# Kernel optimization log

Measured on AMD Instinct MI355X. Metric: run time of the kernel, lower is better.

The kernel has to match this reference:

```python
import jax, jax.numpy as jnp
import numpy as np

B, DEC, F = 64, 12, 32        # batch, decoder steps, decoder feature size
L, H = 2, 512                 # gru layers, hidden size
E, T = 96, 4                  # encoder seq len, target size


def gru_cell(x, h, Wi, Wh, bi, bh):
    # PyTorch GRUCell math
    gi = x @ Wi.T + bi
    gh = h @ Wh.T + bh
    i_r, i_z, i_n = jnp.split(gi, 3, axis=-1)
    h_r, h_z, h_n = jnp.split(gh, 3, axis=-1)
    r = jax.nn.sigmoid(i_r + h_r)
    z = jax.nn.sigmoid(i_z + h_z)
    n = jnp.tanh(i_n + r * h_n)
    return (1.0 - z) * n + z * h


def setup_inputs() -> dict:
    key = jax.random.key(0)
    ks = jax.random.split(key, 12)
    s = lambda k, shape: jax.random.normal(k, shape, jnp.float32) * 0.02
    return {
        "inputs": jax.random.normal(ks[0], (B, DEC, F), jnp.float32),
        "hidden": jax.random.normal(ks[1], (L, B, H), jnp.float32) * 0.1,
        "enc_outputs": jax.random.normal(ks[2], (B, E, H), jnp.float32),
        "target_indices": jnp.arange(T, dtype=jnp.int32),
        "W_attn": s(ks[3], (H, 2 * H)),
        "b_attn": jnp.zeros((H,), jnp.float32),
        "v_attn": s(ks[4], (H,)),
        "gru_Wi0": s(ks[5], (3 * H, F + H)),
        "gru_Wh0": s(ks[6], (3 * H, H)),
        "gru_bi0": jnp.zeros((3 * H,), jnp.float32),
        "gru_bh0": jnp.zeros((3 * H,), jnp.float32),
        "gru_Wi1": s(ks[7], (3 * H, H)),
        "gru_Wh1": s(ks[8], (3 * H, H)),
        "gru_bi1": jnp.zeros((3 * H,), jnp.float32),
        "gru_bh1": jnp.zeros((3 * H,), jnp.float32),
        "W_out": s(ks[9], (T, 2 * H + F)),
        "b_out": jnp.zeros((T,), jnp.float32),
    }


def reference(inputs, hidden, enc_outputs, target_indices,
              W_attn, b_attn, v_attn,
              gru_Wi0, gru_Wh0, gru_bi0, gru_bh0,
              gru_Wi1, gru_Wh1, gru_bi1, gru_bh1,
              W_out, b_out):
    Hs = hidden.shape[-1]
    Wa_h, Wa_e = W_attn[:, :Hs], W_attn[:, Hs:]
    # encoder projection of the attn linear is constant over timesteps
    enc_proj = jnp.einsum('beh,gh->beg', enc_outputs, Wa_e)  # [B,E,H]
    layers = ((gru_Wi0, gru_Wh0, gru_bi0, gru_bh0),
              (gru_Wi1, gru_Wh1, gru_bi1, gru_bh1))

    def step(carry, x_t):
        h, cur = carry                     # h: [L,B,H], cur: [B,F]
        hl = h[-1]                         # final-layer hidden [B,H]
        energy = jnp.tanh(enc_proj + (hl @ Wa_h.T + b_attn)[:, None, :])
        w = jax.nn.softmax(energy @ v_attn, axis=1)          # [B,E]
        ws = jnp.einsum('be,beh->bh', w, enc_outputs)        # [B,H]
        x = jnp.concatenate([cur, ws], axis=-1)              # [B,F+H]
        new_h = []
        for l, (Wi, Wh, bi, bh) in enumerate(layers):
            hn = gru_cell(x, h[l], Wi, Wh, bi, bh)
            new_h.append(hn)
            x = hn
        out = jnp.concatenate([x, ws, cur], axis=-1) @ W_out.T + b_out  # [B,T]
        nxt = x_t.at[:, target_indices].set(out)  # feed prediction back
        return (jnp.stack(new_h), nxt), out

    xs = jnp.swapaxes(inputs, 0, 1)  # [DEC,B,F]
    (_, _), outs = jax.lax.scan(step, (hidden, inputs[:, 0, :]), xs)
    return jnp.swapaxes(outs, 0, 1)  # [B,DEC,T]
```

## Files before the change

kernel.cpp:

```cpp
#include <hip/hip_runtime.h>
#include <hip/hip_fp16.h>

#define NB   64
#define NDEC 12
#define NF   32
#define NH   512
#define NE   96
#define NT   4
#define KI0  (NF + NH)
#define KOUT (2*NH + NF)

typedef _Float16 half8_t __attribute__((ext_vector_type(8)));
typedef float   float4_t __attribute__((ext_vector_type(4)));

__device__ __forceinline__ float fast_tanh(float x) {
    x = fminf(fmaxf(x, -15.f), 15.f);
    float e = __expf(2.f * x);
    return (e - 1.f) / (e + 1.f);
}
__device__ __forceinline__ float fast_sig(float x) {
    return 1.f / (1.f + __expf(-x));
}

__global__ __launch_bounds__(256) void k_prep(
    const float* __restrict__ Wi0, const float* __restrict__ Wh0,
    const float* __restrict__ Wi1, const float* __restrict__ Wh1,
    const float* __restrict__ Wout, const float* __restrict__ Wattn,
    const float* __restrict__ hidden, const float* __restrict__ inputs,
    __half* __restrict__ Wi0h, __half* __restrict__ Wh0h,
    __half* __restrict__ Wi1h, __half* __restrict__ Wh1h,
    __half* __restrict__ Wouth, __half* __restrict__ WahH,
    __half* __restrict__ WaeH,
    float* __restrict__ h0row, float* __restrict__ h1row,
    __half* __restrict__ h0h, __half* __restrict__ h1h,
    __half* __restrict__ xcat_h)
{
    int i = blockIdx.x*256 + threadIdx.x;
    const int n0 = 1536*KI0, n1 = 1536*512, n4 = 4*KOUT, n5 = 512*512;
    if (i < n0) { Wi0h[i] = __float2half_rn(Wi0[i]); return; }  i -= n0;
    if (i < n1) { Wh0h[i] = __float2half_rn(Wh0[i]); return; }  i -= n1;
    if (i < n1) { Wi1h[i] = __float2half_rn(Wi1[i]); return; }  i -= n1;
    if (i < n1) { Wh1h[i] = __float2half_rn(Wh1[i]); return; }  i -= n1;
    if (i < n4) { Wouth[i] = __float2half_rn(Wout[i]); return; } i -= n4;
    if (i < n5) {
        int g = i >> 9, k = i & 511;
        WahH[i] = __float2half_rn(Wattn[(size_t)g*1024 + k]);
        return;
    }
    i -= n5;
    if (i < n5) {
        int g = i >> 9, k = i & 511;
        WaeH[i] = __float2half_rn(Wattn[(size_t)g*1024 + 512 + k]);
        return;
    }
    i -= n5;
    if (i < NB*NH) {
        int b = i >> 9, k = i & 511;
        float v0 = hidden[b*NH + k];
        float v1 = hidden[NB*NH + b*NH + k];
        h0row[b*NH + k] = v0;  h0h[b*NH + k] = __float2half_rn(v0);
        h1row[b*NH + k] = v1;  h1h[b*NH + k] = __float2half_rn(v1);
        return;
    }
    i -= NB*NH;
    if (i < NB*NF) {
        int b = i >> 5, k = i & 31;
        xcat_h[(size_t)b*KI0 + k] = __float2half_rn(inputs[b*NDEC*NF + k]);
    }
}

__global__ __launch_bounds__(256) void k_encproj(const float* __restrict__ enc,
                                                 const __half* __restrict__ WaeH,
                                                 __half* __restrict__ encph) {
    int x = blockIdx.x;
    int by = x >> 3, bx = x & 7;
    int t = threadIdx.x, w = t >> 6, lane = t & 63;
    int mr = lane & 15, kq = lane >> 4;
    int m = by*64 + w*16 + mr;
    const float* arow = enc + (size_t)m*NH;
    float4_t acc[4] = {{0.f,0.f,0.f,0.f},{0.f,0.f,0.f,0.f},
                       {0.f,0.f,0.f,0.f},{0.f,0.f,0.f,0.f}};
    for (int kb = 0; kb < NH; kb += 32) {
        int k = kb + kq*8;
        float4 a0 = *(const float4*)(arow + k);
        float4 a1 = *(const float4*)(arow + k + 4);
        half8_t a;
        a[0] = (_Float16)a0.x; a[1] = (_Float16)a0.y;
        a[2] = (_Float16)a0.z; a[3] = (_Float16)a0.w;
        a[4] = (_Float16)a1.x; a[5] = (_Float16)a1.y;
        a[6] = (_Float16)a1.z; a[7] = (_Float16)a1.w;
        #pragma unroll
        for (int j = 0; j < 4; ++j) {
            int n = bx*64 + j*16 + mr;
            half8_t b = *(const half8_t*)(WaeH + (size_t)n*NH + k);
            acc[j] = __builtin_amdgcn_mfma_f32_16x16x32_f16(a, b, acc[j], 0, 0, 0);
        }
    }
    #pragma unroll
    for (int j = 0; j < 4; ++j) {
        int col = bx*64 + j*16 + mr;
        #pragma unroll
        for (int r = 0; r < 4; ++r) {
            int row = by*64 + w*16 + kq*4 + r;
            encph[(size_t)row*NH + col] = __float2half_rn(acc[j][r]);
        }
    }
}

__global__ __launch_bounds__(256) void k_gemA(
    const float* __restrict__ inputs, const int* __restrict__ tgt,
    const __half* __restrict__ WahH, const float* __restrict__ battn,
    const __half* __restrict__ Wouth, const float* __restrict__ bout,
    const __half* __restrict__ Wh0h, const __half* __restrict__ Wh1h,
    const __half* __restrict__ h0h, const __half* __restrict__ h1h,
    __half* __restrict__ xcat_h,
    float* __restrict__ attcT,
    float* __restrict__ ghb,
    float* __restrict__ out,
    int s, int att_on)
{
    int blk = blockIdx.x, t = threadIdx.x;
    int w = t >> 6, lane = t & 63;
    int mr = lane & 15, kq = lane >> 4;
    int gA = att_on ? 896 : 0;
    __shared__ float parts[4][16][17];

    if (blk < gA) {
        int sblk = (blk & 7)*112 + (blk >> 3);
        const __half* arow;
        const __half* brow;
        float* gdst = nullptr;
        int is_att = 0, rt16 = 0, b0 = 0;
        if (sblk < 128) {
            int rt = sblk >> 2, bq = sblk & 3;
            rt16 = rt*16; b0 = bq*16;
            arow = WahH + (size_t)(rt16 + mr)*NH;
            brow = h1h + (size_t)(b0 + mr)*NH;
            is_att = 1;
        } else {
            int gw = sblk - 128;
            int rt = gw >> 2, bq = gw & 3;
            int layer = (rt >= 96) ? 1 : 0;
            int rloc = (rt - layer*96) * 16;
            const __half* Wh = layer ? Wh1h : Wh0h;
            const __half* Xh = layer ? h1h : h0h;
            arow = Wh + (size_t)(rloc + mr)*NH;
            brow = Xh + (size_t)(bq*16 + mr)*NH;
            gdst = ghb + ((size_t)layer*3*NH + rloc)*NB + bq*16;
        }
        float bat = is_att ? battn[rt16 + (t & 15)] : 0.f;
        int kb0 = w*128 + kq*8;
        half8_t a0 = *(const half8_t*)(arow + kb0);
        half8_t b0v = *(const half8_t*)(brow + kb0);
        half8_t a1 = *(const half8_t*)(arow + kb0 + 32);
        half8_t b1 = *(const half8_t*)(brow + kb0 + 32);
        half8_t a2 = *(const half8_t*)(arow + kb0 + 64);
        half8_t b2 = *(const half8_t*)(brow + kb0 + 64);
        half8_t a3 = *(const half8_t*)(arow + kb0 + 96);
        half8_t b3 = *(const half8_t*)(brow + kb0 + 96);
        float4_t acc = {0.f,0.f,0.f,0.f};
        acc = __builtin_amdgcn_mfma_f32_16x16x32_f16(a0, b0v, acc, 0, 0, 0);
        acc = __builtin_amdgcn_mfma_f32_16x16x32_f16(a1, b1, acc, 0, 0, 0);
        acc = __builtin_amdgcn_mfma_f32_16x16x32_f16(a2, b2, acc, 0, 0, 0);
        acc = __builtin_amdgcn_mfma_f32_16x16x32_f16(a3, b3, acc, 0, 0, 0);
        #pragma unroll
        for (int r = 0; r < 4; ++r) parts[w][kq*4 + r][mr] = acc[r];
        __syncthreads();
        if (is_att) {
            int jl = t & 15, bl = t >> 4;
            float v = parts[0][jl][bl] + parts[1][jl][bl]
                    + parts[2][jl][bl] + parts[3][jl][bl];
            attcT[(size_t)(b0 + bl)*NH + rt16 + jl] = v + bat;
        } else {
            int jl = t >> 4, bl = t & 15;
            float v = parts[0][jl][bl] + parts[1][jl][bl]
                    + parts[2][jl][bl] + parts[3][jl][bl];
            gdst[(size_t)jl*NB + bl] = v;
        }
        return;
    }

    if (s == 0) return;
    int bq = w;
    int b = bq*16 + mr;
    const __half* h1b = h1h + (size_t)b*NH;
    const __half* xcb = xcat_h + (size_t)b*KI0;
    int ar = (mr < 4) ? mr : 3;
    const __half* arow = Wouth + (size_t)ar*KOUT;
    float4_t acc = {0.f,0.f,0.f,0.f};
    for (int kb = 0; kb < KOUT; kb += 32) {
        int k = kb + kq*8;
        half8_t a = *(const half8_t*)(arow + k);
        const __half* bp = (k < NH)   ? (h1b + k)
                         : (k < 2*NH) ? (xcb + NF + (k - NH))
                                      : (xcb + (k - 2*NH));
        half8_t bb = *(const half8_t*)bp;
        acc = __builtin_amdgcn_mfma_f32_16x16x32_f16(a, bb, acc, 0, 0, 0);
    }
    float o0 = __shfl(acc[0], mr) + bout[0];
    float o1 = __shfl(acc[1], mr) + bout[1];
    float o2 = __shfl(acc[2], mr) + bout[2];
    float o3 = __shfl(acc[3], mr) + bout[3];
    if (kq == 0) {
        *(float4*)(out + (size_t)b*(NDEC*NT) + (s-1)*NT) = make_float4(o0,o1,o2,o3);
    }
    if (s < NDEC) {
        int t0 = tgt[0], t1 = tgt[1], t2 = tgt[2], t3 = tgt[3];
        const float* ip = inputs + (size_t)b*(NDEC*NF) + (s-1)*NF;
        half8_t hv;
        #pragma unroll
        for (int i = 0; i < 8; ++i) {
            int f = kq*8 + i;
            float v = ip[f];
            v = (f == t0) ? o0 : (f == t1) ? o1 : (f == t2) ? o2 : (f == t3) ? o3 : v;
            hv[i] = (_Float16)__float2half_rn(v);
        }
        *(half8_t*)(xcat_h + (size_t)b*KI0 + kq*8) = hv;
    }
}

__global__ __launch_bounds__(1024) void k_soft(
    const float* __restrict__ vattn,
    const float* __restrict__ attcT,
    const __half* __restrict__ encph, const float* __restrict__ enc,
    __half* __restrict__ xcat_h)
{
    int b = blockIdx.x, t = threadIdx.x;
    int lane = t & 63, widx = t >> 6;
    __shared__ float vs[NH], atts[NH];
    __shared__ float pes[NE], combA[NH], combB[NH];
    __shared__ float invD_sh;

    if (t < NH) { vs[t] = vattn[t]; atts[t] = attcT[(size_t)b*NH + t]; }

    float er[48];
    {
        int k = t & 511, half = t >> 9;
        const float* eb = enc + ((size_t)b*NE + half*48)*NH + k;
        #pragma unroll
        for (int e = 0; e < 48; ++e) er[e] = eb[(size_t)e*NH];
    }
    __syncthreads();

    {
        float ar[8], vr[8];
        #pragma unroll
        for (int i = 0; i < 8; ++i) { ar[i] = atts[lane*8 + i]; vr[i] = vs[lane*8 + i]; }
        for (int it = 0; it < 6; ++it) {
            int e = widx + it*16;
            const __half* ep = encph + ((size_t)(b*NE + e))*NH + lane*8;
            uint4 u = *(const uint4*)ep;
            __half2 p0 = *(__half2*)&u.x, p1 = *(__half2*)&u.y;
            __half2 p2 = *(__half2*)&u.z, p3 = *(__half2*)&u.w;
            float2 f0 = __half22float2(p0), f1 = __half22float2(p1);
            float2 f2 = __half22float2(p2), f3 = __half22float2(p3);
            float sacc;
            sacc  = fast_tanh(f0.x + ar[0]) * vr[0];
            sacc += fast_tanh(f0.y + ar[1]) * vr[1];
            sacc += fast_tanh(f1.x + ar[2]) * vr[2];
            sacc += fast_tanh(f1.y + ar[3]) * vr[3];
            sacc += fast_tanh(f2.x + ar[4]) * vr[4];
            sacc += fast_tanh(f2.y + ar[5]) * vr[5];
            sacc += fast_tanh(f3.x + ar[6]) * vr[6];
            sacc += fast_tanh(f3.y + ar[7]) * vr[7];
            #pragma unroll
            for (int off = 32; off; off >>= 1) sacc += __shfl_down(sacc, off);
            if (lane == 0) pes[e] = __expf(sacc);
        }
    }
    __syncthreads();

    if (t < 64) {
        float v = pes[t] + ((t < 32) ? pes[64 + t] : 0.f);
        #pragma unroll
        for (int off = 32; off; off >>= 1) v += __shfl_down(v, off);
        if (t == 0) invD_sh = 1.f / v;
    }
    __syncthreads();

    {
        int k = t & 511, half = t >> 9;
        float acc = 0.f;
        #pragma unroll
        for (int e = 0; e < 48; ++e) acc += pes[half*48 + e] * er[e];
        if (half == 0) combA[k] = acc; else combB[k] = acc;
    }
    __syncthreads();
    if (t < NH) {
        float v = (combA[t] + combB[t]) * invD_sh;
        xcat_h[(size_t)b*KI0 + NF + t] = __float2half_rn(v);
    }
}

__global__ __launch_bounds__(768) void k_gru(
    const __half* __restrict__ Wi,
    const float* __restrict__ bi, const float* __restrict__ bh,
    const __half* __restrict__ xh, int K,
    const float* __restrict__ ghbL,
    const float* __restrict__ hold,
    float* __restrict__ hnew,
    __half* __restrict__ hnewh)
{
    int blk = blockIdx.x, t = threadIdx.x;
    int w = t >> 6, lane = t & 63;
    int mr = lane & 15, kq = lane >> 4;
    int sblk = (blk & 7)*16 + (blk >> 3);
    int jg = sblk >> 2, bq = sblk & 3;
    int j0 = jg*16, b0 = bq*16;
    __shared__ float parts[3][4][16][17];

    float ghr = 0.f, ghz = 0.f, ghn = 0.f, hp = 0.f;
    float biR = 0.f, bhR = 0.f, biZ = 0.f, bhZ = 0.f, biN = 0.f, bhN = 0.f;
    if (t < 256) {
        int jl = t >> 4, bl = t & 15;
        int j = j0 + jl, b = b0 + bl;
        ghr = ghbL[(size_t)(0*NH + j)*NB + b];
        ghz = ghbL[(size_t)(1*NH + j)*NB + b];
        ghn = ghbL[(size_t)(2*NH + j)*NB + b];
        hp  = hold[(size_t)b*NH + j];
        biR = bi[j];        bhR = bh[j];
        biZ = bi[NH + j];   bhZ = bh[NH + j];
        biN = bi[2*NH + j]; bhN = bh[2*NH + j];
    }

    int gate = w >> 2, c = w & 3;
    int nsteps = K >> 5;
    int rem = nsteps & 3;
    int base = c*(nsteps >> 2) + ((c < rem) ? c : rem);
    int cnt  = (nsteps >> 2) + ((c < rem) ? 1 : 0);
    const __half* arow = Wi + (size_t)(gate*NH + j0 + mr)*K;
    const __half* brow = xh + (size_t)(b0 + mr)*K;
    float4_t acc = {0.f,0.f,0.f,0.f};
    for (int i2 = 0; i2 < cnt; ++i2) {
        int kb = (base + i2)*32;
        half8_t a = *(const half8_t*)(arow + kb + kq*8);
        half8_t b = *(const half8_t*)(brow + kb + kq*8);
        acc = __builtin_amdgcn_mfma_f32_16x16x32_f16(a, b, acc, 0, 0, 0);
    }
    #pragma unroll
    for (int r = 0; r < 4; ++r) parts[gate][c][kq*4 + r][mr] = acc[r];
    __syncthreads();

    if (t < 256) {
        int jl = t >> 4, bl = t & 15;
        int j = j0 + jl, b = b0 + bl;
        float S0 = parts[0][0][jl][bl] + parts[0][1][jl][bl]
                 + parts[0][2][jl][bl] + parts[0][3][jl][bl];
        float S1 = parts[1][0][jl][bl] + parts[1][1][jl][bl]
                 + parts[1][2][jl][bl] + parts[1][3][jl][bl];
        float S2 = parts[2][0][jl][bl] + parts[2][1][jl][bl]
                 + parts[2][2][jl][bl] + parts[2][3][jl][bl];
        float r = fast_sig(S0 + ghr + biR + bhR);
        float z = fast_sig(S1 + ghz + biZ + bhZ);
        float n = fast_tanh(S2 + biN + r*(ghn + bhN));
        float hv = (1.f - z)*n + z*hp;
        hnew[(size_t)b*NH + j] = hv;
        hnewh[(size_t)b*NH + j] = __float2half_rn(hv);
    }
}

extern "C" void kernel_launch(void* const* d_in, const int* in_sizes, int n_in,
                              void* d_out, int out_size, void* d_ws, size_t ws_size,
                              hipStream_t stream) {
    const float* inputs = (const float*)d_in[0];
    const float* hidden = (const float*)d_in[1];
    const float* enc    = (const float*)d_in[2];
    const int*   tgt    = (const int*)d_in[3];
    const float* Wattn  = (const float*)d_in[4];
    const float* battn  = (const float*)d_in[5];
    const float* vattn  = (const float*)d_in[6];
    const float* Wi0    = (const float*)d_in[7];
    const float* Wh0    = (const float*)d_in[8];
    const float* bi0    = (const float*)d_in[9];
    const float* bh0    = (const float*)d_in[10];
    const float* Wi1    = (const float*)d_in[11];
    const float* Wh1    = (const float*)d_in[12];
    const float* bi1    = (const float*)d_in[13];
    const float* bh1    = (const float*)d_in[14];
    const float* Wout   = (const float*)d_in[15];
    const float* bout   = (const float*)d_in[16];
    float* out = (float*)d_out;

    float* h0row  = (float*)d_ws;
    float* h1row  = h0row + NB*NH;
    float* ghb    = h1row + NB*NH;
    float* attcT  = ghb + 2*3*NH*NB;
    __half* Wi0h  = (__half*)(attcT + NB*NH);
    __half* Wh0h  = Wi0h + 1536*KI0;
    __half* Wi1h  = Wh0h + 1536*NH;
    __half* Wh1h  = Wi1h + 1536*NH;
    __half* Wouth = Wh1h + 1536*NH;
    __half* WahH  = Wouth + 4*KOUT;
    __half* WaeH  = WahH + NH*NH;
    __half* h0h   = WaeH + NH*NH;
    __half* h1h   = h0h + NB*NH;
    __half* xcat_h= h1h + NB*NH;
    __half* encph = xcat_h + NB*KI0;

    const int prep_n = 1536*KI0 + 3*1536*NH + 4*KOUT + 2*NH*NH + NB*NH + NB*NF;
    k_prep<<<(prep_n + 255)/256, 256, 0, stream>>>(
        Wi0, Wh0, Wi1, Wh1, Wout, Wattn, hidden, inputs,
        Wi0h, Wh0h, Wi1h, Wh1h, Wouth, WahH, WaeH,
        h0row, h1row, h0h, h1h, xcat_h);
    k_encproj<<<768, 256, 0, stream>>>(enc, WaeH, encph);

    for (int s = 0; s < NDEC; ++s) {
        k_gemA<<<(s == 0) ? 896 : 897, 256, 0, stream>>>(
            inputs, tgt, WahH, battn, Wouth, bout, Wh0h, Wh1h,
            h0h, h1h, xcat_h, attcT, ghb, out, s, 1);
        k_soft<<<NB, 1024, 0, stream>>>(vattn, attcT, encph, enc, xcat_h);
        k_gru<<<128, 768, 0, stream>>>(Wi0h, bi0, bh0,
                                       xcat_h, KI0,
                                       ghb,
                                       h0row, h0row, h0h);
        k_gru<<<128, 768, 0, stream>>>(Wi1h, bi1, bh1,
                                       h0h, NH,
                                       ghb + 3*NH*NB,
                                       h1row, h1row, h1h);
    }
    k_gemA<<<1, 256, 0, stream>>>(
        inputs, tgt, WahH, battn, Wouth, bout, Wh0h, Wh1h,
        h0h, h1h, xcat_h, attcT, ghb, out, NDEC, 0);
}
```

Measured before the change: 533.4 us.

## Move hidden-gate GEMMs and output head into softmax kernel with double-buffered xcat

The per-step work is rebalanced across kernels. The attention projection becomes its own small 32-block kernel. The recurrent gate GEMMs (Wh·h) and the output/feedback block now run as extra blocks inside the softmax kernel, so they overlap with the attention softmax. xcat is double-buffered so the output head can read the previous step's concatenated input while the softmax blocks write the current one. The critical path gets shorter, at the cost of an extra launch and 1024-thread blocks doing small GEMM tiles.

```diff
diff --git a/kernel.cpp b/kernel.cpp
--- a/kernel.cpp
+++ b/kernel.cpp
@@ -33,7 +33,7 @@
     __half* __restrict__ WaeH,
     float* __restrict__ h0row, float* __restrict__ h1row,
     __half* __restrict__ h0h, __half* __restrict__ h1h,
-    __half* __restrict__ xcat_h)
+    __half* __restrict__ xcat0)
 {
     int i = blockIdx.x*256 + threadIdx.x;
     const int n0 = 1536*KI0, n1 = 1536*512, n4 = 4*KOUT, n5 = 512*512;
@@ -65,7 +65,7 @@
     i -= NB*NH;
     if (i < NB*NF) {
         int b = i >> 5, k = i & 31;
-        xcat_h[(size_t)b*KI0 + k] = __float2half_rn(inputs[b*NDEC*NF + k]);
+        xcat0[(size_t)b*KI0 + k] = __float2half_rn(inputs[b*NDEC*NF + k]);
     }
 }
 
@@ -107,51 +107,81 @@
     }
 }
 
-__global__ __launch_bounds__(256) void k_gemA(
-    const float* __restrict__ inputs, const int* __restrict__ tgt,
+__global__ __launch_bounds__(1024) void k_att(
     const __half* __restrict__ WahH, const float* __restrict__ battn,
-    const __half* __restrict__ Wouth, const float* __restrict__ bout,
-    const __half* __restrict__ Wh0h, const __half* __restrict__ Wh1h,
-    const __half* __restrict__ h0h, const __half* __restrict__ h1h,
-    __half* __restrict__ xcat_h,
-    float* __restrict__ attcT,
-    float* __restrict__ ghb,
-    float* __restrict__ out,
-    int s, int att_on)
+    const __half* __restrict__ h1h,
+    float* __restrict__ attcT)
 {
     int blk = blockIdx.x, t = threadIdx.x;
     int w = t >> 6, lane = t & 63;
     int mr = lane & 15, kq = lane >> 4;
-    int gA = att_on ? 896 : 0;
-    __shared__ float parts[4][16][17];
-
-    if (blk < gA) {
-        int sblk = (blk & 7)*112 + (blk >> 3);
-        const __half* arow;
-        const __half* brow;
-        float* gdst = nullptr;
-        int is_att = 0, rt16 = 0, b0 = 0;
-        if (sblk < 128) {
-            int rt = sblk >> 2, bq = sblk & 3;
-            rt16 = rt*16; b0 = bq*16;
-            arow = WahH + (size_t)(rt16 + mr)*NH;
-            brow = h1h + (size_t)(b0 + mr)*NH;
-            is_att = 1;
-        } else {
-            int gw = sblk - 128;
-            int rt = gw >> 2, bq = gw & 3;
-            int layer = (rt >= 96) ? 1 : 0;
-            int rloc = (rt - layer*96) * 16;
-            const __half* Wh = layer ? Wh1h : Wh0h;
-            const __half* Xh = layer ? h1h : h0h;
-            arow = Wh + (size_t)(rloc + mr)*NH;
-            brow = Xh + (size_t)(bq*16 + mr)*NH;
-            gdst = ghb + ((size_t)layer*3*NH + rloc)*NB + bq*16;
-        }
-        float bat = is_att ? battn[rt16 + (t & 15)] : 0.f;
-        int kb0 = w*128 + kq*8;
+    int rt = (blk & 7)*4 + (blk >> 3);
+    int rt16 = rt*16;
+    int bq = w >> 2, wq = w & 3;
+    __shared__ float parts[4][4][16][17];
+
+    float bat = battn[rt16 + (t & 15)];
+    const __half* arow = WahH + (size_t)(rt16 + mr)*NH;
+    const __half* brow = h1h + (size_t)(bq*16 + mr)*NH;
+    int kb0 = wq*128 + kq*8;
+    half8_t a0 = *(const half8_t*)(arow + kb0);
+    half8_t b0 = *(const half8_t*)(brow + kb0);
+    half8_t a1 = *(const half8_t*)(arow + kb0 + 32);
+    half8_t b1 = *(const half8_t*)(brow + kb0 + 32);
+    half8_t a2 = *(const half8_t*)(arow + kb0 + 64);
+    half8_t b2 = *(const half8_t*)(brow + kb0 + 64);
+    half8_t a3 = *(const half8_t*)(arow + kb0 + 96);
+    half8_t b3 = *(const half8_t*)(brow + kb0 + 96);
+    float4_t acc = {0.f,0.f,0.f,0.f};
+    acc = __builtin_amdgcn_mfma_f32_16x16x32_f16(a0, b0, acc, 0, 0, 0);
+    acc = __builtin_amdgcn_mfma_f32_16x16x32_f16(a1, b1, acc, 0, 0, 0);
+    acc = __builtin_amdgcn_mfma_f32_16x16x32_f16(a2, b2, acc, 0, 0, 0);
+    acc = __builtin_amdgcn_mfma_f32_16x16x32_f16(a3, b3, acc, 0, 0, 0);
+    #pragma unroll
+    for (int r = 0; r < 4; ++r) parts[bq][wq][kq*4 + r][mr] = acc[r];
+    __syncthreads();
+
+    int sub = t >> 8, tt = t & 255;
+    int jl = tt & 15, bl = tt >> 4;
+    float v = parts[sub][0][jl][bl] + parts[sub][1][jl][bl]
+            + parts[sub][2][jl][bl] + parts[sub][3][jl][bl];
+    attcT[(size_t)(sub*16 + bl)*NH + rt16 + jl] = v + bat;
+}
+
+__global__ __launch_bounds__(1024) void k_soft(
+    const float* __restrict__ inputs, const int* __restrict__ tgt,
+    const float* __restrict__ vattn,
+    const float* __restrict__ attcT,
+    const __half* __restrict__ encph, const float* __restrict__ enc,
+    const __half* __restrict__ Wouth, const float* __restrict__ bout,
+    const __half* __restrict__ Wh0h, const __half* __restrict__ Wh1h,
+    const __half* __restrict__ h0h, const __half* __restrict__ h1h,
+    float* __restrict__ ghb,
+    const __half* __restrict__ xcatP,
+    __half* __restrict__ xcatC,
+    float* __restrict__ out, int s)
+{
+    int blk = blockIdx.x, t = threadIdx.x;
+    int lane = t & 63, widx = t >> 6;
+    __shared__ float vs[NH], atts[NH];
+    __shared__ float pes[NE], combA[NH], combB[NH];
+    __shared__ float invD_sh;
+    __shared__ float parts[4][4][16][17];
+
+    if (blk >= 64 && blk < 256) {
+        int gblk = blk - 64;
+        int rt = (gblk & 7)*24 + (gblk >> 3);
+        int layer = (rt >= 96) ? 1 : 0;
+        int rloc = (rt - layer*96) * 16;
+        int bq = widx >> 2, wq = widx & 3;
+        int mr = lane & 15, kq = lane >> 4;
+        const __half* Wh = layer ? Wh1h : Wh0h;
+        const __half* Xh = layer ? h1h : h0h;
+        const __half* arow = Wh + (size_t)(rloc + mr)*NH;
+        const __half* brow = Xh + (size_t)(bq*16 + mr)*NH;
+        int kb0 = wq*128 + kq*8;
         half8_t a0 = *(const half8_t*)(arow + kb0);
-        half8_t b0v = *(const half8_t*)(brow + kb0);
+        half8_t b0 = *(const half8_t*)(brow + kb0);
         half8_t a1 = *(const half8_t*)(arow + kb0 + 32);
         half8_t b1 = *(const half8_t*)(brow + kb0 + 32);
         half8_t a2 = *(const half8_t*)(arow + kb0 + 64);
@@ -159,52 +189,46 @@
         half8_t a3 = *(const half8_t*)(arow + kb0 + 96);
         half8_t b3 = *(const half8_t*)(brow + kb0 + 96);
         float4_t acc = {0.f,0.f,0.f,0.f};
-        acc = __builtin_amdgcn_mfma_f32_16x16x32_f16(a0, b0v, acc, 0, 0, 0);
+        acc = __builtin_amdgcn_mfma_f32_16x16x32_f16(a0, b0, acc, 0, 0, 0);
         acc = __builtin_amdgcn_mfma_f32_16x16x32_f16(a1, b1, acc, 0, 0, 0);
         acc = __builtin_amdgcn_mfma_f32_16x16x32_f16(a2, b2, acc, 0, 0, 0);
         acc = __builtin_amdgcn_mfma_f32_16x16x32_f16(a3, b3, acc, 0, 0, 0);
         #pragma unroll
-        for (int r = 0; r < 4; ++r) parts[w][kq*4 + r][mr] = acc[r];
+        for (int r = 0; r < 4; ++r) parts[bq][wq][kq*4 + r][mr] = acc[r];
         __syncthreads();
-        if (is_att) {
-            int jl = t & 15, bl = t >> 4;
-            float v = parts[0][jl][bl] + parts[1][jl][bl]
-                    + parts[2][jl][bl] + parts[3][jl][bl];
-            attcT[(size_t)(b0 + bl)*NH + rt16 + jl] = v + bat;
-        } else {
-            int jl = t >> 4, bl = t & 15;
-            float v = parts[0][jl][bl] + parts[1][jl][bl]
-                    + parts[2][jl][bl] + parts[3][jl][bl];
-            gdst[(size_t)jl*NB + bl] = v;
-        }
+        int sub = t >> 8, tt = t & 255;
+        int jl = tt >> 4, bl = tt & 15;
+        float v = parts[sub][0][jl][bl] + parts[sub][1][jl][bl]
+                + parts[sub][2][jl][bl] + parts[sub][3][jl][bl];
+        ghb[((size_t)layer*3*NH + rloc + jl)*NB + sub*16 + bl] = v;
         return;
     }
 
-    if (s == 0) return;
-    int bq = w;
-    int b = bq*16 + mr;
-    const __half* h1b = h1h + (size_t)b*NH;
-    const __half* xcb = xcat_h + (size_t)b*KI0;
-    int ar = (mr < 4) ? mr : 3;
-    const __half* arow = Wouth + (size_t)ar*KOUT;
-    float4_t acc = {0.f,0.f,0.f,0.f};
-    for (int kb = 0; kb < KOUT; kb += 32) {
-        int k = kb + kq*8;
-        half8_t a = *(const half8_t*)(arow + k);
-        const __half* bp = (k < NH)   ? (h1b + k)
-                         : (k < 2*NH) ? (xcb + NF + (k - NH))
-                                      : (xcb + (k - 2*NH));
-        half8_t bb = *(const half8_t*)bp;
-        acc = __builtin_amdgcn_mfma_f32_16x16x32_f16(a, bb, acc, 0, 0, 0);
-    }
-    float o0 = __shfl(acc[0], mr) + bout[0];
-    float o1 = __shfl(acc[1], mr) + bout[1];
-    float o2 = __shfl(acc[2], mr) + bout[2];
-    float o3 = __shfl(acc[3], mr) + bout[3];
-    if (kq == 0) {
-        *(float4*)(out + (size_t)b*(NDEC*NT) + (s-1)*NT) = make_float4(o0,o1,o2,o3);
-    }
-    if (s < NDEC) {
+    if (blk == 256) {
+        if (s == 0 || widx >= 4) return;
+        int mr = lane & 15, kq = lane >> 4;
+        int b = widx*16 + mr;
+        const __half* h1b = h1h + (size_t)b*NH;
+        const __half* xcb = xcatP + (size_t)b*KI0;
+        int ar = (mr < 4) ? mr : 3;
+        const __half* arow = Wouth + (size_t)ar*KOUT;
+        float4_t acc = {0.f,0.f,0.f,0.f};
+        for (int kb = 0; kb < KOUT; kb += 32) {
+            int k = kb + kq*8;
+            half8_t a = *(const half8_t*)(arow + k);
+            const __half* bp = (k < NH)   ? (h1b + k)
+                             : (k < 2*NH) ? (xcb + NF + (k - NH))
+                                          : (xcb + (k - 2*NH));
+            half8_t bb = *(const half8_t*)bp;
+            acc = __builtin_amdgcn_mfma_f32_16x16x32_f16(a, bb, acc, 0, 0, 0);
+        }
+        float o0 = __shfl(acc[0], mr) + bout[0];
+        float o1 = __shfl(acc[1], mr) + bout[1];
+        float o2 = __shfl(acc[2], mr) + bout[2];
+        float o3 = __shfl(acc[3], mr) + bout[3];
+        if (kq == 0) {
+            *(float4*)(out + (size_t)b*(NDEC*NT) + (s-1)*NT) = make_float4(o0,o1,o2,o3);
+        }
         int t0 = tgt[0], t1 = tgt[1], t2 = tgt[2], t3 = tgt[3];
         const float* ip = inputs + (size_t)b*(NDEC*NF) + (s-1)*NF;
         half8_t hv;
@@ -215,22 +239,11 @@
             v = (f == t0) ? o0 : (f == t1) ? o1 : (f == t2) ? o2 : (f == t3) ? o3 : v;
             hv[i] = (_Float16)__float2half_rn(v);
         }
-        *(half8_t*)(xcat_h + (size_t)b*KI0 + kq*8) = hv;
-    }
-}
-
-__global__ __launch_bounds__(1024) void k_soft(
-    const float* __restrict__ vattn,
-    const float* __restrict__ attcT,
-    const __half* __restrict__ encph, const float* __restrict__ enc,
-    __half* __restrict__ xcat_h)
-{
-    int b = blockIdx.x, t = threadIdx.x;
-    int lane = t & 63, widx = t >> 6;
-    __shared__ float vs[NH], atts[NH];
-    __shared__ float pes[NE], combA[NH], combB[NH];
-    __shared__ float invD_sh;
-
+        *(half8_t*)(xcatC + (size_t)b*KI0 + kq*8) = hv;
+        return;
+    }
+
+    int b = blk;
     if (t < NH) { vs[t] = vattn[t]; atts[t] = attcT[(size_t)b*NH + t]; }
 
     float er[48];
@@ -288,7 +301,7 @@
     __syncthreads();
     if (t < NH) {
         float v = (combA[t] + combB[t]) * invD_sh;
-        xcat_h[(size_t)b*KI0 + NF + t] = __float2half_rn(v);
+        xcatC[(size_t)b*KI0 + NF + t] = __float2half_rn(v);
     }
 }
 
@@ -356,6 +369,38 @@
         float hv = (1.f - z)*n + z*hp;
         hnew[(size_t)b*NH + j] = hv;
         hnewh[(size_t)b*NH + j] = __float2half_rn(hv);
+    }
+}
+
+__global__ __launch_bounds__(256) void k_outp(
+    const __half* __restrict__ Wouth, const float* __restrict__ bout,
+    const __half* __restrict__ h1h, const __half* __restrict__ xcatP,
+    float* __restrict__ out)
+{
+    int t = threadIdx.x;
+    int w = t >> 6, lane = t & 63;
+    int mr = lane & 15, kq = lane >> 4;
+    int b = w*16 + mr;
+    const __half* h1b = h1h + (size_t)b*NH;
+    const __half* xcb = xcatP + (size_t)b*KI0;
+    int ar = (mr < 4) ? mr : 3;
+    const __half* arow = Wouth + (size_t)ar*KOUT;
+    float4_t acc = {0.f,0.f,0.f,0.f};
+    for (int kb = 0; kb < KOUT; kb += 32) {
+        int k = kb + kq*8;
+        half8_t a = *(const half8_t*)(arow + k);
+        const __half* bp = (k < NH)   ? (h1b + k)
+                         : (k < 2*NH) ? (xcb + NF + (k - NH))
+                                      : (xcb + (k - 2*NH));
+        half8_t bb = *(const half8_t*)bp;
+        acc = __builtin_amdgcn_mfma_f32_16x16x32_f16(a, bb, acc, 0, 0, 0);
+    }
+    float o0 = __shfl(acc[0], mr) + bout[0];
+    float o1 = __shfl(acc[1], mr) + bout[1];
+    float o2 = __shfl(acc[2], mr) + bout[2];
+    float o3 = __shfl(acc[3], mr) + bout[3];
+    if (kq == 0) {
+        *(float4*)(out + (size_t)b*(NDEC*NT) + (NDEC-1)*NT) = make_float4(o0,o1,o2,o3);
     }
 }
 
@@ -394,23 +439,26 @@
     __half* WaeH  = WahH + NH*NH;
     __half* h0h   = WaeH + NH*NH;
     __half* h1h   = h0h + NB*NH;
-    __half* xcat_h= h1h + NB*NH;
-    __half* encph = xcat_h + NB*KI0;
+    __half* xcat  = h1h + NB*NH;
+    __half* encph = xcat + 2*NB*KI0;
 
     const int prep_n = 1536*KI0 + 3*1536*NH + 4*KOUT + 2*NH*NH + NB*NH + NB*NF;
     k_prep<<<(prep_n + 255)/256, 256, 0, stream>>>(
         Wi0, Wh0, Wi1, Wh1, Wout, Wattn, hidden, inputs,
         Wi0h, Wh0h, Wi1h, Wh1h, Wouth, WahH, WaeH,
-        h0row, h1row, h0h, h1h, xcat_h);
+        h0row, h1row, h0h, h1h, xcat);
     k_encproj<<<768, 256, 0, stream>>>(enc, WaeH, encph);
 
     for (int s = 0; s < NDEC; ++s) {
-        k_gemA<<<(s == 0) ? 896 : 897, 256, 0, stream>>>(
-            inputs, tgt, WahH, battn, Wouth, bout, Wh0h, Wh1h,
-            h0h, h1h, xcat_h, attcT, ghb, out, s, 1);
-        k_soft<<<NB, 1024, 0, stream>>>(vattn, attcT, encph, enc, xcat_h);
+        int par = s & 1;
+        __half* xcatC = xcat + par*NB*KI0;
+        __half* xcatP = xcat + (par^1)*NB*KI0;
+        k_att<<<32, 1024, 0, stream>>>(WahH, battn, h1h, attcT);
+        k_soft<<<257, 1024, 0, stream>>>(
+            inputs, tgt, vattn, attcT, encph, enc, Wouth, bout,
+            Wh0h, Wh1h, h0h, h1h, ghb, xcatP, xcatC, out, s);
         k_gru<<<128, 768, 0, stream>>>(Wi0h, bi0, bh0,
-                                       xcat_h, KI0,
+                                       xcatC, KI0,
                                        ghb,
                                        h0row, h0row, h0h);
         k_gru<<<128, 768, 0, stream>>>(Wi1h, bi1, bh1,
@@ -418,7 +466,5 @@
                                        ghb + 3*NH*NB,
                                        h1row, h1row, h1h);
     }
-    k_gemA<<<1, 256, 0, stream>>>(
-        inputs, tgt, WahH, battn, Wouth, bout, Wh0h, Wh1h,
-        h0h, h1h, xcat_h, attcT, ghb, out, NDEC, 0);
-}
+    k_outp<<<1, 256, 0, stream>>>(Wouth, bout, h1h, xcat + (NB*KI0), out);
+}
```

Result: faster. 485.5 us, median of 2 (-9.0%).
